# Optimization experiments

Measured on AMD Instinct MI355X. Metric: run time of the kernel, lower is better.

Reference implementation:

```python
import jax, jax.numpy as jnp
import numpy as np

B, T, C, H = 8, 1024, 768, 12
D = C // H  # head_dim = 64

def _rope_tables(seq_len, d, base=10000.0):
    inv_freq = 1.0 / (base ** (jnp.arange(0, d, 2, dtype=jnp.float32) / d))  # [d/2]
    freqs = jnp.outer(jnp.arange(seq_len, dtype=jnp.float32), inv_freq)      # [T, d/2]
    return jnp.cos(freqs), jnp.sin(freqs)

def _apply_rotary(x, cos, sin):
    # x: [B,T,H,D]; cos/sin: [1,T,1,D/2]
    d = x.shape[-1] // 2
    x1, x2 = x[..., :d], x[..., d:]
    return jnp.concatenate([x1 * cos + x2 * sin, -x1 * sin + x2 * cos], axis=-1)

def setup_inputs() -> dict:
    key = jax.random.key(0)
    k1, k2, k3 = jax.random.split(key, 3)
    x = jax.random.normal(k1, (B, T, C), dtype=jnp.float32)
    w_qkv = jax.random.normal(k2, (3 * C, C), dtype=jnp.float32) * (C ** -0.5)
    w_proj = jax.random.normal(k3, (C, C), dtype=jnp.float32) * (C ** -0.5)
    return {"x": x, "w_qkv": w_qkv, "w_proj": w_proj}

def reference(x, w_qkv, w_proj):
    Bb, Tt, Cc = x.shape
    qkv = x @ w_qkv.T                                   # [B,T,3C]
    q, k, v = jnp.split(qkv, 3, axis=2)
    q = q.reshape(Bb, Tt, H, D)
    k = k.reshape(Bb, Tt, H, D)
    v = v.reshape(Bb, Tt, H, D)
    cos, sin = _rope_tables(Tt, D)
    cos = cos[None, :, None, :]
    sin = sin[None, :, None, :]
    q = _apply_rotary(q, cos, sin)
    k = _apply_rotary(k, cos, sin)
    scale = 1.0 / jnp.sqrt(jnp.float32(D))
    scores = jnp.einsum('bthd,bshd->bhts', q, k) * scale  # [B,H,T,T]
    causal = jnp.tril(jnp.ones((Tt, Tt), dtype=bool))
    scores = jnp.where(causal[None, None], scores, jnp.finfo(scores.dtype).min)
    p = jax.nn.softmax(scores, axis=-1)
    y = jnp.einsum('bhts,bshd->bthd', p, v).reshape(Bb, Tt, Cc)
    return y @ w_proj.T
```

## Files before the change

kernel.cpp:

```cpp
#include <hip/hip_runtime.h>
#include <hip/hip_bf16.h>

#define Bb 8
#define Tt 1024
#define Cc 768
#define Hh 12
#define Dd 64
#define M_ROWS (Bb * Tt)
#define QKV_N (3 * Cc)

typedef __attribute__((ext_vector_type(8))) short s16x8;
typedef __attribute__((ext_vector_type(4))) short s16x4;
typedef __attribute__((ext_vector_type(4))) float f32x4;

#define AS1 __attribute__((address_space(1)))
#define AS3 __attribute__((address_space(3)))

template <int V> struct IC { static constexpr int value = V; };

static __device__ __forceinline__ short f2bf(float f) {
    union { float f; unsigned u; } v; v.f = f;
    unsigned r = (v.u + 0x7fffu + ((v.u >> 16) & 1u)) >> 16;
    return (short)r;
}
static __device__ __forceinline__ unsigned pkt(float hi, float lo) {
    union { float f; unsigned u; } a, b; a.f = hi; b.f = lo;
    return __builtin_amdgcn_perm(a.u, b.u, 0x07060302u);
}

static __device__ __forceinline__ void cast8(const float* __restrict__ in,
                                             short* __restrict__ out, int i) {
    const float4 a = ((const float4*)in)[i * 2];
    const float4 b = ((const float4*)in)[i * 2 + 1];
    s16x8 f;
    f[0] = f2bf(a.x); f[1] = f2bf(a.y); f[2] = f2bf(a.z); f[3] = f2bf(a.w);
    f[4] = f2bf(b.x); f[5] = f2bf(b.y); f[6] = f2bf(b.z); f[7] = f2bf(b.w);
    ((s16x8*)out)[i] = f;
}

#define S1 (M_ROWS * Cc / 8)
#define S2 (QKV_N * Cc / 8)
#define S3 (Cc * Cc / 8)
#define SROPE (Tt * 32)
#define PREP_THREADS (S1 + S2 + S3 + SROPE)

__global__ __launch_bounds__(256) void prep_kernel(const float* __restrict__ x,
                                                   const float* __restrict__ wqkv,
                                                   const float* __restrict__ wproj,
                                                   short* __restrict__ xb,
                                                   short* __restrict__ wqkvb,
                                                   short* __restrict__ wprojb,
                                                   float2* __restrict__ cs) {
    int idx = blockIdx.x * blockDim.x + threadIdx.x;
    if (idx < S1) { cast8(x, xb, idx); return; }
    idx -= S1;
    if (idx < S2) {
        int row = idx / 96;
        int c8  = idx - row * 96;
        int q2 = (row >> 4) & 3;
        int src = (row < 2 * Cc && (q2 == 1 || q2 == 2)) ? (row ^ 0x30) : row;
        const float4 a = ((const float4*)(wqkv + (size_t)src * Cc))[c8 * 2];
        const float4 b = ((const float4*)(wqkv + (size_t)src * Cc))[c8 * 2 + 1];
        s16x8 f;
        f[0] = f2bf(a.x); f[1] = f2bf(a.y); f[2] = f2bf(a.z); f[3] = f2bf(a.w);
        f[4] = f2bf(b.x); f[5] = f2bf(b.y); f[6] = f2bf(b.z); f[7] = f2bf(b.w);
        ((s16x8*)wqkvb)[idx] = f;
        return;
    }
    idx -= S2;
    if (idx < S3) { cast8(wproj, wprojb, idx); return; }
    idx -= S3;
    {
        int t = idx >> 5, i = idx & 31;
        float inv_freq = exp2f(-0.41524101186092037f * (float)i);
        float fr = (float)t * inv_freq;
        float2 v; v.x = cosf(fr); v.y = sinf(fr);
        cs[idx] = v;
    }
}

template <int MODE, int TN>
__global__ __launch_bounds__(256, 3) void gemm_nt_mfma(const short* __restrict__ A,
                                                       const short* __restrict__ B,
                                                       void* __restrict__ Cout,
                                                       const float2* __restrict__ cs,
                                                       int M, int N, int K, int nblocks) {
    __shared__ short As[2][128 * 32];
    __shared__ short Bs[2][TN * 32];
    constexpr int NTW = TN / 32;

    const int wave = threadIdx.x >> 6;
    const int lane = threadIdx.x & 63;
    const int l16  = lane & 15;
    const int quad = lane >> 4;
    const int wr = wave >> 1;
    const int wc = wave & 1;

    const int mb8  = (M >> 7) >> 3;
    const int xcd  = blockIdx.x & 7;
    const int slot = blockIdx.x >> 3;
    const int bm = (xcd * mb8 + slot / nblocks) * 128;
    const int bn = (slot % nblocks) * TN;

    f32x4 acc[4][NTW] = {};

    auto stage = [&](int k0, int buf) {
#pragma unroll
        for (int j = 0; j < 2; j++) {
            const int D = j * 256 + wave * 64 + lane;
            const int G = D >> 3;
            const int s = (G << 3) | ((D & 7) ^ (G & 7));
            const int m = s >> 2, c4 = (s & 3) * 8;
            __builtin_amdgcn_global_load_lds(
                (const AS1 unsigned*)(A + (size_t)(bm + m) * K + k0 + c4),
                (AS3 unsigned*)&As[buf][(j * 256 + wave * 64) * 8], 16, 0, 0);
        }
        constexpr int BCH = TN * 4;
#pragma unroll
        for (int j = 0; j < (BCH + 255) / 256; j++) {
            if (BCH % 256 == 0 || j * 256 + wave * 64 < BCH) {
                const int D = j * 256 + wave * 64 + lane;
                const int G = D >> 3;
                const int s = (G << 3) | ((D & 7) ^ (G & 7));
                const int m = s >> 2, c4 = (s & 3) * 8;
                __builtin_amdgcn_global_load_lds(
                    (const AS1 unsigned*)(B + (size_t)(bn + m) * K + k0 + c4),
                    (AS3 unsigned*)&Bs[buf][(j * 256 + wave * 64) * 8], 16, 0, 0);
            }
        }
    };

    const int nIter = K >> 5;
    stage(0, 0);
    for (int kt = 0; kt < nIter; kt++) {
        const int buf = kt & 1;
        __syncthreads();
        if (kt + 1 < nIter) stage((kt + 1) << 5, buf ^ 1);

        s16x8 af[4];
#pragma unroll
        for (int mt = 0; mt < 4; mt++) {
            const int m = wr * 64 + mt * 16 + l16;
            const int d = ((m & 1) * 4 + quad) ^ ((m >> 1) & 7);
            af[mt] = *(const s16x8*)&As[buf][(m >> 1) * 64 + d * 8];
        }
#pragma unroll
        for (int nt = 0; nt < NTW; nt++) {
            const int n = wc * (TN / 2) + nt * 16 + l16;
            const int d = ((n & 1) * 4 + quad) ^ ((n >> 1) & 7);
            s16x8 bf = *(const s16x8*)&Bs[buf][(n >> 1) * 64 + d * 8];
#pragma unroll
            for (int mt = 0; mt < 4; mt++)
                acc[mt][nt] = __builtin_amdgcn_mfma_f32_16x16x32_bf16(
                    af[mt], bf, acc[mt][nt], 0, 0, 0);
        }
    }

    if constexpr (MODE == 0) {
#pragma unroll
        for (int mt = 0; mt < 4; mt++)
#pragma unroll
            for (int r = 0; r < 4; r++) {
                const size_t row = bm + wr * 64 + mt * 16 + quad * 4 + r;
#pragma unroll
                for (int nt = 0; nt < NTW; nt++)
                    ((float*)Cout)[row * N + bn + wc * (TN / 2) + nt * 16 + l16] =
                        acc[mt][nt][r];
            }
    } else {
        const bool is_v = (bn >= 2 * Cc);
        if (is_v) {
#pragma unroll
            for (int mt = 0; mt < 4; mt++)
#pragma unroll
                for (int r = 0; r < 4; r++) {
                    const size_t row = bm + wr * 64 + mt * 16 + quad * 4 + r;
#pragma unroll
                    for (int nt = 0; nt < NTW; nt++)
                        ((short*)Cout)[row * N + bn + wc * (TN / 2) + nt * 16 + l16] =
                            f2bf(acc[mt][nt][r]);
                }
        } else {
            const float scale = (bn < Cc) ? 0.125f : 1.0f;
#pragma unroll
            for (int mt = 0; mt < 4; mt++) {
#pragma unroll
                for (int r = 0; r < 4; r++) {
                    const int row = bm + wr * 64 + mt * 16 + quad * 4 + r;
                    const int t = row & (Tt - 1);
                    short* cp = (short*)Cout + (size_t)row * N + bn + wc * (TN / 2);
#pragma unroll
                    for (int p = 0; p < NTW; p += 2) {
                        const int g = wc * NTW + p;
                        const int i0 = ((g & 2) ? 16 : 0) + l16;
                        const float2 c0 = cs[t * 32 + i0];
                        const float x1 = acc[mt][p][r];
                        const float x2 = acc[mt][p + 1][r];
                        cp[p * 16 + l16]        = f2bf((x1 * c0.x + x2 * c0.y) * scale);
                        cp[(p + 1) * 16 + l16]  = f2bf((-x1 * c0.y + x2 * c0.x) * scale);
                    }
                }
            }
        }
    }
}

#define QBM 256
#define QBN 288

__global__ __launch_bounds__(512, 2) void qkv_gemm_8ph(const short* __restrict__ A,
                                                       const short* __restrict__ Bw,
                                                       short* __restrict__ Cq,
                                                       const float2* __restrict__ cs) {
    __shared__ short As[4][QBM * 32];
    __shared__ short Bs[4][QBN * 32];

    const int tid  = threadIdx.x;
    const int wave = tid >> 6;
    const int lane = tid & 63;
    const int l16  = lane & 15;
    const int quad = lane >> 4;
    const int wr   = wave >> 1;
    const int wc   = wave & 1;

    const int xcd = blockIdx.x & 7;
    const int bn  = xcd * QBN;
    const int bm  = (blockIdx.x >> 3) * QBM;
    const int gt0 = xcd * 18;

    int aoff0, boff0, boffR;
    {
        const int G = tid >> 3;
        const int s = (G << 3) | ((tid & 7) ^ (G & 7));
        aoff0 = (s >> 2) * Cc + (s & 3) * 8;
        boff0 = aoff0;
    }
    {
        const int D = 1024 + (wave & 1) * 64 + lane;
        const int G = D >> 3;
        const int s = (G << 3) | ((D & 7) ^ (G & 7));
        boffR = (s >> 2) * Cc + (s & 3) * 8;
    }
    const short* Ag = A + (size_t)bm * Cc;
    const short* Bg = Bw + (size_t)bn * Cc;

    const int mA = wr * 64 + l16;
    const int abase = (mA >> 1) * 128 + ((((mA & 1) * 4 + quad) ^ ((mA >> 1) & 7)) * 16);
    const int nB = wc * 144 + l16;
    const int bbase = (nB >> 1) * 128 + ((((nB & 1) * 4 + quad) ^ ((nB >> 1) & 7)) * 16);

    f32x4 acc[4][9] = {};

#define STG_A(J, SB, K0) __builtin_amdgcn_global_load_lds(                    \
        (const AS1 unsigned*)(Ag + aoff0 + (J) * (128 * Cc) + (K0)),          \
        (AS3 unsigned*)&As[SB][((J) * 512 + wave * 64) * 8], 16, 0, 0)
#define STG_B(J, SB, K0) __builtin_amdgcn_global_load_lds(                    \
        (const AS1 unsigned*)(Bg + boff0 + (J) * (128 * Cc) + (K0)),          \
        (AS3 unsigned*)&Bs[SB][((J) * 512 + wave * 64) * 8], 16, 0, 0)
#define STG_BR(SB, K0) __builtin_amdgcn_global_load_lds(                      \
        (const AS1 unsigned*)(Bg + boffR + (K0)),                             \
        (AS3 unsigned*)&Bs[SB][(1024 + (wave & 1) * 64) * 8], 16, 0, 0)

#pragma unroll
    for (int t = 0; t < 3; t++) {
        const int k0 = t << 5;
        STG_A(0, t, k0); STG_A(1, t, k0);
        STG_B(0, t, k0); STG_B(1, t, k0); STG_BR(t, k0);
    }
    asm volatile("s_waitcnt vmcnt(10)" ::: "memory");
    __builtin_amdgcn_s_barrier();
    asm volatile("" ::: "memory");

    for (int kt = 0; kt < 24; kt++) {
        const int buf  = kt & 3;
        const int sb   = (kt + 3) & 3;
        const int k0n  = (kt + 3) << 5;
        const bool st  = (kt < 21);
        const char* ap = (const char*)&As[buf][0];
        const char* bp = (const char*)&Bs[buf][0];

        if (st) { STG_A(0, sb, k0n); STG_A(1, sb, k0n); STG_B(0, sb, k0n); }
        s16x8 bf[9];
#pragma unroll
        for (int nt = 0; nt < 9; nt++)
            bf[nt] = *(const s16x8*)(bp + bbase + nt * 1024);
        {
            s16x8 a0 = *(const s16x8*)(ap + abase);
            s16x8 a1 = *(const s16x8*)(ap + abase + 1024);
            __builtin_amdgcn_s_setprio(1);
#pragma unroll
            for (int nt = 0; nt < 9; nt++) {
                acc[0][nt] = __builtin_amdgcn_mfma_f32_16x16x32_bf16(a0, bf[nt], acc[0][nt], 0, 0, 0);
                acc[1][nt] = __builtin_amdgcn_mfma_f32_16x16x32_bf16(a1, bf[nt], acc[1][nt], 0, 0, 0);
            }
            __builtin_amdgcn_s_setprio(0);
        }
        if (st) { STG_B(1, sb, k0n); STG_BR(sb, k0n); }
        {
            s16x8 a2 = *(const s16x8*)(ap + abase + 2048);
            s16x8 a3 = *(const s16x8*)(ap + abase + 3072);
            __builtin_amdgcn_s_setprio(1);
#pragma unroll
            for (int nt = 0; nt < 9; nt++) {
                acc[2][nt] = __builtin_amdgcn_mfma_f32_16x16x32_bf16(a2, bf[nt], acc[2][nt], 0, 0, 0);
                acc[3][nt] = __builtin_amdgcn_mfma_f32_16x16x32_bf16(a3, bf[nt], acc[3][nt], 0, 0, 0);
            }
            __builtin_amdgcn_s_setprio(0);
        }
        if (kt < 23) {
            if (kt < 21)       asm volatile("s_waitcnt vmcnt(10)" ::: "memory");
            else if (kt == 21) asm volatile("s_waitcnt vmcnt(5)"  ::: "memory");
            else               asm volatile("s_waitcnt vmcnt(0)"  ::: "memory");
            __builtin_amdgcn_s_barrier();
            asm volatile("" ::: "memory");
        }
    }

    __builtin_amdgcn_s_barrier();
    asm volatile("" ::: "memory");
    float* scr = (float*)&As[0][0];
    if (wc == 0) {
#pragma unroll
        for (int mt = 0; mt < 4; mt++)
#pragma unroll
            for (int r = 0; r < 4; r++)
                scr[((wr * 4 + mt) * 16 + quad * 4 + r) * 16 + l16] = acc[mt][8][r];
    } else {
#pragma unroll
        for (int mt = 0; mt < 4; mt++)
#pragma unroll
            for (int r = 0; r < 4; r++)
                scr[(((4 + wr) * 4 + mt) * 16 + quad * 4 + r) * 16 + l16] = acc[mt][0][r];
    }
    __builtin_amdgcn_s_barrier();
    asm volatile("" ::: "memory");

    auto write_epi = [&](auto WCC) {
        constexpr int WC = decltype(WCC)::value;
        constexpr int PO = WC ? 0 : 8;
#pragma unroll
        for (int mt = 0; mt < 4; mt++) {
#pragma unroll
            for (int r = 0; r < 4; r++) {
                const int row = bm + wr * 64 + mt * 16 + quad * 4 + r;
                const int t = row & (Tt - 1);
                short* cp = Cq + (size_t)row * QKV_N + bn + WC * 144;
#pragma unroll
                for (int pp = 0; pp < 4; pp++) {
                    constexpr int PBASE = WC;
                    const int p = PBASE + 2 * pp;
                    const int g = gt0 + WC * 9 + p;
                    float x1, x2;
                    switch (pp) {
                        case 0: x1 = acc[mt][PBASE + 0][r]; x2 = acc[mt][PBASE + 1][r]; break;
                        case 1: x1 = acc[mt][PBASE + 2][r]; x2 = acc[mt][PBASE + 3][r]; break;
                        case 2: x1 = acc[mt][PBASE + 4][r]; x2 = acc[mt][PBASE + 5][r]; break;
                        default: x1 = acc[mt][PBASE + 6][r]; x2 = acc[mt][PBASE + 7][r]; break;
                    }
                    if (g < 96) {
                        const int i0 = ((g & 2) ? 16 : 0) + l16;
                        const float2 c0 = cs[t * 32 + i0];
                        const float sc = (g < 48) ? 0.125f : 1.0f;
                        cp[p * 16 + l16]       = f2bf((x1 * c0.x + x2 * c0.y) * sc);
                        cp[(p + 1) * 16 + l16] = f2bf((-x1 * c0.y + x2 * c0.x) * sc);
                    } else {
                        cp[p * 16 + l16]       = f2bf(x1);
                        cp[(p + 1) * 16 + l16] = f2bf(x2);
                    }
                }
                const float xo = acc[mt][PO][r];
                const float xp = scr[((((WC ^ 1) * 4 + wr) * 4 + mt) * 16 + quad * 4 + r) * 16 + l16];
                const int ge = gt0 + 8;
                if constexpr (WC == 0) {
                    if (ge < 96) {
                        const int i0 = ((ge & 2) ? 16 : 0) + l16;
                        const float2 c0 = cs[t * 32 + i0];
                        const float sc = (ge < 48) ? 0.125f : 1.0f;
                        cp[8 * 16 + l16] = f2bf((xo * c0.x + xp * c0.y) * sc);
                    } else {
                        cp[8 * 16 + l16] = f2bf(xo);
                    }
                } else {
                    if (ge < 96) {
                        const int i0 = ((ge & 2) ? 16 : 0) + l16;
                        const float2 c0 = cs[t * 32 + i0];
                        const float sc = (ge < 48) ? 0.125f : 1.0f;
                        cp[l16] = f2bf((-xp * c0.y + xo * c0.x) * sc);
                    } else {
                        cp[l16] = f2bf(xo);
                    }
                }
            }
        }
    };
    if (wc == 0) write_epi(IC<0>{});
    else         write_epi(IC<1>{});
#undef STG_A
#undef STG_B
#undef STG_BR
}

#define KSP 72
#define VSP 72

__global__ __launch_bounds__(256, 3) void flash_attn(const short* __restrict__ qkv,
                                                     short* __restrict__ y) {
    __shared__ short Ks[2][64 * KSP];
    __shared__ short Vs[2][64 * VSP];

    const int wave = threadIdx.x >> 6;
    const int lane = threadIdx.x & 63;
    const int l16  = lane & 15;
    const int quad = lane >> 4;

    const int pair = blockIdx.x / 96;
    const int bh   = blockIdx.x % 96;
    const int h = bh % Hh;
    const int b = bh / Hh;
    const int qa_blk = pair;
    const int qb_blk = 15 - pair;
    const int q0a = qa_blk * 64 + wave * 16;
    const int q0b = qb_blk * 64 + wave * 16;

    s16x8 qfa[2], qfb[2];
    {
        const short* qpa = qkv + (size_t)(b * Tt + q0a + l16) * QKV_N + h * Dd + quad * 8;
        const short* qpb = qkv + (size_t)(b * Tt + q0b + l16) * QKV_N + h * Dd + quad * 8;
        qfa[0] = *(const s16x8*)qpa;  qfa[1] = *(const s16x8*)(qpa + 32);
        qfb[0] = *(const s16x8*)qpb;  qfb[1] = *(const s16x8*)(qpb + 32);
    }

    f32x4 oa[4] = {}, ob[4] = {};
    float la = 0.f, lb = 0.f;

    const int krow = threadIdx.x >> 2;
    const int kd0  = (threadIdx.x & 3) * 16;
    const int key2 = (threadIdx.x & 31) * 2;
    const int dv0  = (threadIdx.x >> 5) * 8;

    s16x8 pk0, pk1, pv0, pv1;
    auto load_tile = [&](int kbase) {
        const short* kp = qkv + (size_t)(b * Tt + kbase + krow) * QKV_N + Cc + h * Dd + kd0;
        pk0 = *(const s16x8*)kp;
        pk1 = *(const s16x8*)(kp + 8);
        const short* vp = qkv + (size_t)(b * Tt + kbase + key2) * QKV_N + 2 * Cc + h * Dd + dv0;
        pv0 = *(const s16x8*)vp;
        pv1 = *(const s16x8*)(vp + QKV_N);
    };
    auto store_tile = [&](int buf) {
        *(s16x8*)&Ks[buf][krow * KSP + kd0]     = pk0;
        *(s16x8*)&Ks[buf][krow * KSP + kd0 + 8] = pk1;
#pragma unroll
        for (int j = 0; j < 8; j++) {
            ushort2 w; w.x = (unsigned short)pv0[j]; w.y = (unsigned short)pv1[j];
            *(ushort2*)&Vs[buf][(dv0 + j) * VSP + key2] = w;
        }
    };

    auto process_pair = [&](int buf, int kbase, bool mask_a) {
        short* pwb = &Ks[buf ^ 1][wave * 16 * KSP];
        short* pwa = &Vs[buf ^ 1][wave * 16 * VSP];
        f32x4 eb[4], ea[4];
#pragma unroll
        for (int g = 0; g < 4; g++) {
            s16x8 kf0 = *(const s16x8*)&Ks[buf][(g * 16 + l16) * KSP + quad * 8];
            s16x8 kf1 = *(const s16x8*)&Ks[buf][(g * 16 + l16) * KSP + 32 + quad * 8];
            f32x4 zb = {}, za = {};
            zb = __builtin_amdgcn_mfma_f32_16x16x32_bf16(kf0, qfb[0], zb, 0, 0, 0);
            zb = __builtin_amdgcn_mfma_f32_16x16x32_bf16(kf1, qfb[1], zb, 0, 0, 0);
            za = __builtin_amdgcn_mfma_f32_16x16x32_bf16(kf0, qfa[0], za, 0, 0, 0);
            za = __builtin_amdgcn_mfma_f32_16x16x32_bf16(kf1, qfa[1], za, 0, 0, 0);
            eb[g] = zb; ea[g] = za;
        }
        float rsb = 0.f, rsa = 0.f;
#pragma unroll
        for (int g = 0; g < 4; g++) {
#pragma unroll
            for (int r = 0; r < 4; r++) {
                float pb = __expf(eb[g][r]); rsb += pb; eb[g][r] = pb;
                float pa = __expf(ea[g][r]);
                if (mask_a) pa = (kbase + g * 16 + quad * 4 + r <= q0a + l16) ? pa : 0.0f;
                rsa += pa; ea[g][r] = pa;
            }
            uint2 ub, ua;
            ub.x = pkt(eb[g][1], eb[g][0]); ub.y = pkt(eb[g][3], eb[g][2]);
            ua.x = pkt(ea[g][1], ea[g][0]); ua.y = pkt(ea[g][3], ea[g][2]);
            *(uint2*)&pwb[l16 * KSP + g * 16 + quad * 4] = ub;
            *(uint2*)&pwa[l16 * VSP + g * 16 + quad * 4] = ua;
        }
        lb += rsb; la += rsa;
#pragma unroll
        for (int c = 0; c < 2; c++) {
            s16x8 pbb = *(const s16x8*)&pwb[l16 * KSP + c * 32 + quad * 8];
            s16x8 pba = *(const s16x8*)&pwa[l16 * VSP + c * 32 + quad * 8];
#pragma unroll
            for (int nc = 0; nc < 4; nc++) {
                s16x8 vb = *(const s16x8*)&Vs[buf][(nc * 16 + l16) * VSP + c * 32 + quad * 8];
                ob[nc] = __builtin_amdgcn_mfma_f32_16x16x32_bf16(vb, pbb, ob[nc], 0, 0, 0);
                oa[nc] = __builtin_amdgcn_mfma_f32_16x16x32_bf16(vb, pba, oa[nc], 0, 0, 0);
            }
        }
    };

    auto process_single = [&](int buf, int kbase, bool masked) {
        short* pw = &Ks[buf ^ 1][wave * 16 * KSP];
        f32x4 e[4];
#pragma unroll
        for (int g = 0; g < 4; g++) {
            s16x8 kf0 = *(const s16x8*)&Ks[buf][(g * 16 + l16) * KSP + quad * 8];
            s16x8 kf1 = *(const s16x8*)&Ks[buf][(g * 16 + l16) * KSP + 32 + quad * 8];
            f32x4 z = {};
            z = __builtin_amdgcn_mfma_f32_16x16x32_bf16(kf0, qfb[0], z, 0, 0, 0);
            z = __builtin_amdgcn_mfma_f32_16x16x32_bf16(kf1, qfb[1], z, 0, 0, 0);
            e[g] = z;
        }
        float rs = 0.f;
#pragma unroll
        for (int g = 0; g < 4; g++) {
#pragma unroll
            for (int r = 0; r < 4; r++) {
                float p = __expf(e[g][r]);
                if (masked) p = (kbase + g * 16 + quad * 4 + r <= q0b + l16) ? p : 0.0f;
                rs += p; e[g][r] = p;
            }
            uint2 u;
            u.x = pkt(e[g][1], e[g][0]); u.y = pkt(e[g][3], e[g][2]);
            *(uint2*)&pw[l16 * KSP + g * 16 + quad * 4] = u;
        }
        lb += rs;
#pragma unroll
        for (int c = 0; c < 2; c++) {
            s16x8 pb = *(const s16x8*)&pw[l16 * KSP + c * 32 + quad * 8];
#pragma unroll
            for (int nc = 0; nc < 4; nc++) {
                s16x8 vb = *(const s16x8*)&Vs[buf][(nc * 16 + l16) * VSP + c * 32 + quad * 8];
                ob[nc] = __builtin_amdgcn_mfma_f32_16x16x32_bf16(vb, pb, ob[nc], 0, 0, 0);
            }
        }
    };

    load_tile(0);
    store_tile(0);
    for (int kt = 0; kt <= qb_blk; kt++) {
        __syncthreads();
        const int nb = (kt < qb_blk) ? (kt + 1) * 64 : qb_blk * 64;
        load_tile(nb);
        const int buf = kt & 1;
        const int kbase = kt * 64;
        if (kt <= qa_blk)
            process_pair(buf, kbase, kt == qa_blk);
        else
            process_single(buf, kbase, kt == qb_blk);
        store_tile(buf ^ 1);
    }

    float sa = la; sa += __shfl_xor(sa, 16, 64); sa += __shfl_xor(sa, 32, 64);
    float sb = lb; sb += __shfl_xor(sb, 16, 64); sb += __shfl_xor(sb, 32, 64);
    const float inva = 1.0f / sa;
    const float invb = 1.0f / sb;
    short* ypa = y + (size_t)(b * Tt + q0a + l16) * Cc + h * Dd + quad * 4;
    short* ypb = y + (size_t)(b * Tt + q0b + l16) * Cc + h * Dd + quad * 4;
#pragma unroll
    for (int nc = 0; nc < 4; nc++) {
        s16x4 va, vb2;
#pragma unroll
        for (int r = 0; r < 4; r++) {
            va[r]  = f2bf(oa[nc][r] * inva);
            vb2[r] = f2bf(ob[nc][r] * invb);
        }
        *(s16x4*)&ypa[nc * 16] = va;
        *(s16x4*)&ypb[nc * 16] = vb2;
    }
}

extern "C" void kernel_launch(void* const* d_in, const int* in_sizes, int n_in,
                              void* d_out, int out_size, void* d_ws, size_t ws_size,
                              hipStream_t stream) {
    const float* x      = (const float*)d_in[0];
    const float* w_qkv  = (const float*)d_in[1];
    const float* w_proj = (const float*)d_in[2];
    float* out = (float*)d_out;

    float2* cs    = (float2*)d_ws;
    short* xb     = (short*)(cs + Tt * 32);
    short* wqkvb  = xb + (size_t)M_ROWS * Cc;
    short* wprojb = wqkvb + (size_t)QKV_N * Cc;
    short* qkvb   = wprojb + (size_t)Cc * Cc;
    short* yb     = qkvb + (size_t)M_ROWS * QKV_N;

    prep_kernel<<<PREP_THREADS / 256, 256, 0, stream>>>(
        x, w_qkv, w_proj, xb, wqkvb, wprojb, cs);

    qkv_gemm_8ph<<<256, 512, 0, stream>>>(xb, wqkvb, qkvb, cs);

    flash_attn<<<96 * 8, 256, 0, stream>>>(qkvb, yb);

    gemm_nt_mfma<0, 96><<<512, 256, 0, stream>>>(
        yb, wprojb, out, nullptr, M_ROWS, Cc, Cc, Cc / 96);
}
```

Measured before the change: 182.6 us.

## Shrink QKV GEMM tile to 128x288 with 4 waves and triple buffering

Restructures the QKV projection GEMM from a 256x288 tile with 8 waves and a 4-stage LDS ring to a 128x288 tile with 4 waves and a 3-stage ring, launching 512 blocks instead of 256. The block-to-tile mapping now groups row tiles per XCD instead of column tiles per XCD, so each XCD shares A rows rather than B columns in L2. All stage loads are issued together at the top of each iteration, and the epilogue barrier is simplified. The aim is better occupancy and wave-level parallelism. The cost is less reuse per block and a shallower prefetch pipeline.

Measured after the change: 177.0 us. 3.0% less time.

```diff
diff --git a/kernel.cpp b/kernel.cpp
--- a/kernel.cpp
+++ b/kernel.cpp
@@ -205,15 +205,15 @@
     }
 }
 
-#define QBM 256
+#define QBM 128
 #define QBN 288
 
-__global__ __launch_bounds__(512, 2) void qkv_gemm_8ph(const short* __restrict__ A,
-                                                       const short* __restrict__ Bw,
-                                                       short* __restrict__ Cq,
-                                                       const float2* __restrict__ cs) {
-    __shared__ short As[4][QBM * 32];
-    __shared__ short Bs[4][QBN * 32];
+__global__ __launch_bounds__(256, 2) void qkv_gemm_v3(const short* __restrict__ A,
+                                                      const short* __restrict__ Bw,
+                                                      short* __restrict__ Cq,
+                                                      const float2* __restrict__ cs) {
+    __shared__ short As[3][QBM * 32];
+    __shared__ short Bs[3][QBN * 32];
 
     const int tid  = threadIdx.x;
     const int wave = tid >> 6;
@@ -223,17 +223,17 @@
     const int wr   = wave >> 1;
     const int wc   = wave & 1;
 
-    const int xcd = blockIdx.x & 7;
-    const int bn  = xcd * QBN;
-    const int bm  = (blockIdx.x >> 3) * QBM;
-    const int gt0 = xcd * 18;
-
-    int aoff0, boff0, boffR;
+    const int xcd  = blockIdx.x & 7;
+    const int slot = blockIdx.x >> 3;
+    const int bm   = (xcd * 8 + (slot >> 3)) * QBM;
+    const int bn   = (slot & 7) * QBN;
+    const int gt0  = (slot & 7) * 18;
+
+    int aoff0, boffR;
     {
         const int G = tid >> 3;
         const int s = (G << 3) | ((tid & 7) ^ (G & 7));
         aoff0 = (s >> 2) * Cc + (s & 3) * 8;
-        boff0 = aoff0;
     }
     {
         const int D = 1024 + (wave & 1) * 64 + lane;
@@ -252,34 +252,33 @@
     f32x4 acc[4][9] = {};
 
 #define STG_A(J, SB, K0) __builtin_amdgcn_global_load_lds(                    \
-        (const AS1 unsigned*)(Ag + aoff0 + (J) * (128 * Cc) + (K0)),          \
-        (AS3 unsigned*)&As[SB][((J) * 512 + wave * 64) * 8], 16, 0, 0)
+        (const AS1 unsigned*)(Ag + aoff0 + (J) * (64 * Cc) + (K0)),           \
+        (AS3 unsigned*)&As[SB][((J) * 256 + wave * 64) * 8], 16, 0, 0)
 #define STG_B(J, SB, K0) __builtin_amdgcn_global_load_lds(                    \
-        (const AS1 unsigned*)(Bg + boff0 + (J) * (128 * Cc) + (K0)),          \
-        (AS3 unsigned*)&Bs[SB][((J) * 512 + wave * 64) * 8], 16, 0, 0)
+        (const AS1 unsigned*)(Bg + aoff0 + (J) * (64 * Cc) + (K0)),           \
+        (AS3 unsigned*)&Bs[SB][((J) * 256 + wave * 64) * 8], 16, 0, 0)
 #define STG_BR(SB, K0) __builtin_amdgcn_global_load_lds(                      \
         (const AS1 unsigned*)(Bg + boffR + (K0)),                             \
         (AS3 unsigned*)&Bs[SB][(1024 + (wave & 1) * 64) * 8], 16, 0, 0)
-
-#pragma unroll
-    for (int t = 0; t < 3; t++) {
-        const int k0 = t << 5;
-        STG_A(0, t, k0); STG_A(1, t, k0);
-        STG_B(0, t, k0); STG_B(1, t, k0); STG_BR(t, k0);
-    }
-    asm volatile("s_waitcnt vmcnt(10)" ::: "memory");
+#define STG_ALL(SB, K0) do { STG_A(0, SB, K0); STG_A(1, SB, K0);              \
+        STG_B(0, SB, K0); STG_B(1, SB, K0); STG_B(2, SB, K0);                 \
+        STG_B(3, SB, K0); STG_BR(SB, K0); } while (0)
+
+    STG_ALL(0, 0);
+    STG_ALL(1, 32);
+    asm volatile("s_waitcnt vmcnt(7)" ::: "memory");
     __builtin_amdgcn_s_barrier();
     asm volatile("" ::: "memory");
 
+    int buf = 0;
     for (int kt = 0; kt < 24; kt++) {
-        const int buf  = kt & 3;
-        const int sb   = (kt + 3) & 3;
-        const int k0n  = (kt + 3) << 5;
-        const bool st  = (kt < 21);
+        const int sb  = (buf == 0) ? 2 : buf - 1;
+        const int k0n = (kt + 2) << 5;
         const char* ap = (const char*)&As[buf][0];
         const char* bp = (const char*)&Bs[buf][0];
 
-        if (st) { STG_A(0, sb, k0n); STG_A(1, sb, k0n); STG_B(0, sb, k0n); }
+        if (kt < 22) STG_ALL(sb, k0n);
+
         s16x8 bf[9];
 #pragma unroll
         for (int nt = 0; nt < 9; nt++)
@@ -295,7 +294,6 @@
             }
             __builtin_amdgcn_s_setprio(0);
         }
-        if (st) { STG_B(1, sb, k0n); STG_BR(sb, k0n); }
         {
             s16x8 a2 = *(const s16x8*)(ap + abase + 2048);
             s16x8 a3 = *(const s16x8*)(ap + abase + 3072);
@@ -308,16 +306,14 @@
             __builtin_amdgcn_s_setprio(0);
         }
         if (kt < 23) {
-            if (kt < 21)       asm volatile("s_waitcnt vmcnt(10)" ::: "memory");
-            else if (kt == 21) asm volatile("s_waitcnt vmcnt(5)"  ::: "memory");
-            else               asm volatile("s_waitcnt vmcnt(0)"  ::: "memory");
+            if (kt <= 21) asm volatile("s_waitcnt vmcnt(7)" ::: "memory");
+            else          asm volatile("s_waitcnt vmcnt(0)" ::: "memory");
             __builtin_amdgcn_s_barrier();
             asm volatile("" ::: "memory");
         }
-    }
-
-    __builtin_amdgcn_s_barrier();
-    asm volatile("" ::: "memory");
+        buf = (buf == 2) ? 0 : buf + 1;
+    }
+
     float* scr = (float*)&As[0][0];
     if (wc == 0) {
 #pragma unroll
@@ -330,10 +326,9 @@
         for (int mt = 0; mt < 4; mt++)
 #pragma unroll
             for (int r = 0; r < 4; r++)
-                scr[(((4 + wr) * 4 + mt) * 16 + quad * 4 + r) * 16 + l16] = acc[mt][0][r];
-    }
-    __builtin_amdgcn_s_barrier();
-    asm volatile("" ::: "memory");
+                scr[(((2 + wr) * 4 + mt) * 16 + quad * 4 + r) * 16 + l16] = acc[mt][0][r];
+    }
+    __syncthreads();
 
     auto write_epi = [&](auto WCC) {
         constexpr int WC = decltype(WCC)::value;
@@ -369,7 +364,7 @@
                     }
                 }
                 const float xo = acc[mt][PO][r];
-                const float xp = scr[((((WC ^ 1) * 4 + wr) * 4 + mt) * 16 + quad * 4 + r) * 16 + l16];
+                const float xp = scr[((((WC ^ 1) * 2 + wr) * 4 + mt) * 16 + quad * 4 + r) * 16 + l16];
                 const int ge = gt0 + 8;
                 if constexpr (WC == 0) {
                     if (ge < 96) {
@@ -398,6 +393,7 @@
 #undef STG_A
 #undef STG_B
 #undef STG_BR
+#undef STG_ALL
 }
 
 #define KSP 72
@@ -591,7 +587,7 @@
     prep_kernel<<<PREP_THREADS / 256, 256, 0, stream>>>(
         x, w_qkv, w_proj, xb, wqkvb, wprojb, cs);
 
-    qkv_gemm_8ph<<<256, 512, 0, stream>>>(xb, wqkvb, qkvb, cs);
+    qkv_gemm_v3<<<512, 256, 0, stream>>>(xb, wqkvb, qkvb, cs);
 
     flash_attn<<<96 * 8, 256, 0, stream>>>(qkvb, yb);
 
```
